# Kernel optimization log

Hardware: AMD Instinct MI355X
Metric: run time of the kernel (lower is better)

The kernel has to match this reference:

```python
import jax, jax.numpy as jnp
import numpy as np

# ---- static geometry derived from truncation (matches torch __init__) ----
T = 127
N_LAT_NH = T + 1                                   # 128 NH latitudes
LONS = [20 + 4 * i for i in range(N_LAT_NH)]       # octahedral reduced grid
CUMS = np.concatenate([[0], np.cumsum(np.array(LONS + LONS[::-1]))]).astype(int)
HZW_NH = np.minimum(4 + np.arange(N_LAT_NH), T)    # cubic truncation: m_max = nlon//4 - 1, capped at T
N_LATS_PER_M = np.array([(HZW_NH >= m).sum() for m in range(T + 1)])
L_SYM_FULL = (T + 3) // 2                          # 65 rows before dropping row 0
L_ANT = (T + 2) // 2                               # 64
N_VARS = 128
BATCH, ENS = 4, 1


def _tri_masks():
    """Zero-padded triangular structure of the per-m Legendre matrices."""
    sym = np.zeros((T + 1, L_SYM_FULL, N_LAT_NH), np.float32)
    ant = np.zeros((T + 1, L_ANT, N_LAT_NH), np.float32)
    for m in range(T + 1):
        n_lats = int(N_LATS_PER_M[m])
        ms = (T - m + 3) // 2
        off = L_SYM_FULL - ms
        sym[m, off:, N_LAT_NH - n_lats:] = 1.0
        if (m + 1) % 2 == 1:
            sym[m, off, :] = 0.0
        ma = (T - m + 2) // 2
        off = L_ANT - ma
        ant[m, off:, N_LAT_NH - n_lats:] = 1.0
        if m % 2 == 1:
            ant[m, off, :] = 0.0
    return sym[:, 1:, :], ant   # module drops first symmetric row -> [128,64,128]


def setup_inputs() -> dict:
    key = jax.random.key(0)
    k1, k2, k3 = jax.random.split(key, 3)
    n_grid = int(CUMS[-1])
    x = jax.random.normal(k1, (BATCH, ENS, n_grid, N_VARS), jnp.float32)
    sm, am = _tri_masks()
    # random stand-ins for (gaussian-weight-fused) Legendre polynomials, with the exact
    # triangular zero structure the module builds from ecTrans assets
    symmetric = jax.random.normal(k2, sm.shape, jnp.float32) * jnp.asarray(sm)
    antisymmetric = jax.random.normal(k3, am.shape, jnp.float32) * jnp.asarray(am)
    return {"x": x, "symmetric": symmetric, "antisymmetric": antisymmetric}


def reference(x, symmetric, antisymmetric):
    """Octahedral SHT forward: ragged longitudinal rfft -> hemispheric fold -> per-m Legendre matmuls.

    Returns spectrum [b, e, l, m, vars, 2] (real/imag stacked on last axis).
    """
    n_lat = 2 * N_LAT_NH
    north, south = [], []
    # loop is over structurally distinct (ragged) latitude ring lengths; NH lat i and its
    # SH mirror (lat n_lat-1-i) share nlon/truncation, so batch them in one FFT call.
    for i in range(N_LAT_NH):
        j = n_lat - 1 - i
        nlon = LONS[i]
        xn = x[:, :, CUMS[i]:CUMS[i + 1], :]           # [b,e,nlon,v]
        xs = x[:, :, CUMS[j]:CUMS[j + 1], :]
        xp = jnp.stack([xn, xs], axis=2)               # [b,e,2,nlon,v]
        f = jnp.fft.rfft(xp, axis=3) / nlon            # torch norm='forward'
        m_hi = int(HZW_NH[i]) + 1                      # keep m <= highest zonal wavenumber
        f = f[:, :, :, :m_hi, :]
        f = jnp.pad(f, ((0, 0), (0, 0), (0, 0), (0, T + 1 - m_hi), (0, 0)))
        north.append(f[:, :, 0])
        south.append(f[:, :, 1])                       # index i <-> lat n_lat-1-i: already pole-mirrored
    north = jnp.stack(north, axis=2)                   # [b,e,n_lat_nh,m,v] complex64
    south = jnp.stack(south, axis=2)
    # hemispheric symmetry of Legendre polynomials
    sym = north + south
    anti = north - south
    # per-m truncated Legendre contractions over NH latitudes (n)
    out_s = jnp.einsum('mln,benmv->belmv', symmetric, sym)     # [b,e,64,m,v]
    out_a = jnp.einsum('mln,benmv->belmv', antisymmetric, anti)
    # interleave symmetric (l-m even) and antisymmetric (l-m odd) rows -> full l axis (128)
    spec = jnp.stack([out_s, out_a], axis=3)
    b, e, L, _, M, V = spec.shape
    spec = spec.reshape(b, e, 2 * L, M, V)             # [b,e,l,m,v] complex, lower triangle zeros
    return jnp.stack([spec.real, spec.imag], axis=-1)  # real view [b,e,l,m,v,2]
```

## Files before the change

kernel.cpp:

```cpp
#include <hip/hip_runtime.h>
#include <math.h>

#define NGRID 70144
#define NV 128
#define JT 16
#define VS 64

typedef float f32x4 __attribute__((ext_vector_type(4)));
typedef short short8 __attribute__((ext_vector_type(8)));

__device__ __forceinline__ float4 f4add(float4 a, float4 b){ return make_float4(a.x+b.x, a.y+b.y, a.z+b.z, a.w+b.w); }
__device__ __forceinline__ float4 f4sub(float4 a, float4 b){ return make_float4(a.x-b.x, a.y-b.y, a.z-b.z, a.w-b.w); }

__device__ __forceinline__ unsigned f2bf(float f){
  unsigned u = __float_as_uint(f);
  return (u + 0x7FFFu + ((u>>16)&1u)) >> 16;
}
__device__ __forceinline__ float bf2f(unsigned h){ return __uint_as_float(h<<16); }

__device__ __forceinline__ long twoff_of(int i){
  long off = 0;
  for(int k=0;k<i;k++){
    int mh = (5+k < 128) ? (5+k) : 128;
    off += (long)mh * (long)(11 + 2*k);
  }
  return off;
}

__global__ void fill_tw(float* __restrict__ tw){
  int ring = blockIdx.x, mc = blockIdx.y;
  int N = 20 + 4*ring, H = N/2;
  int mhi = (5+ring < 128) ? (5+ring) : 128;
  int m0 = mc*32;
  if(m0 >= mhi) return;
  int m1 = (m0+32 < mhi) ? (m0+32) : mhi;
  long base = twoff_of(ring);
  int tot = (m1-m0)*(H+1);
  float invN = 1.0f / (float)N;
  for(int idx = threadIdx.x; idx < tot; idx += blockDim.x){
    int m = m0 + idx/(H+1);
    int j = idx % (H+1);
    int p = (m*j) % N;
    float th = 6.2831853071795864f * (float)p * invN;
    float sn, cs;
    __sincosf(th, &sn, &cs);
    long o = (base + (long)(m)*(H+1) + j)*2;
    tw[o]   = cs * invN;
    tw[o+1] = -sn * invN;
  }
}

__global__ __launch_bounds__(256) void dft_fold(const float* __restrict__ x,
                                                const float* __restrict__ tw,
                                                unsigned short* __restrict__ Gh,
                                                unsigned short* __restrict__ Gl){
  int ring = 127 - blockIdx.x;
  int mt = blockIdx.y;
  int b  = blockIdx.z >> 1;
  int vh = blockIdx.z & 1;
  int N = 20 + 4*ring, H = N/2, JC = H+1;
  int mhi = (5+ring < 128) ? (5+ring) : 128;
  int mbase = mt*32;
  if(mbase >= mhi) return;

  __shared__ __align__(16) float cS[JT][VS], sS[JT][VS], cA[JT][VS], sA[JT][VS];
  __shared__ __align__(16) float twl[JT][32][2];

  int tid = threadIdx.x;
  int vl = tid & 63;
  int mg = tid >> 6;
  int v  = vh*64 + vl;

  long twbase = twoff_of(ring);
  long offN = (long)ring*(2*ring+18);
  long a = ring+1;
  long offS = (long)NGRID - a*(2*a+18);
  const float* xn = x + ((long)b*NGRID + offN)*NV + vh*64;
  const float* xs = x + ((long)b*NGRID + offS)*NV + vh*64;

  float aSR[8], aSI[8], aAR[8], aAI[8];
  #pragma unroll
  for(int k=0;k<8;k++){ aSR[k]=0.f; aSI[k]=0.f; aAR[k]=0.f; aAI[k]=0.f; }

  int sjj = tid >> 4;
  int sv4 = (tid & 15) << 2;
  int tmp2 = (tid & 15) << 1;

  for(int j0=0; j0<JC; j0+=JT){
    __syncthreads();
    {
      int j = j0 + sjj;
      float4 z = make_float4(0.f,0.f,0.f,0.f);
      float4 nj=z, sj=z, np=z, sp=z;
      if(j < JC){
        nj = *(const float4*)&xn[(long)j*NV + sv4];
        sj = *(const float4*)&xs[(long)j*NV + sv4];
        if(j > 0 && j < H){
          int jp = N - j;
          np = *(const float4*)&xn[(long)jp*NV + sv4];
          sp = *(const float4*)&xs[(long)jp*NV + sv4];
        }
      }
      float4 e  = f4add(nj, sj);
      float4 o  = f4sub(nj, sj);
      float4 ep = f4add(np, sp);
      float4 op = f4sub(np, sp);
      *(float4*)&cS[sjj][sv4] = f4add(e, ep);
      *(float4*)&sS[sjj][sv4] = f4sub(e, ep);
      *(float4*)&cA[sjj][sv4] = f4add(o, op);
      *(float4*)&sA[sjj][sv4] = f4sub(o, op);
    }
    {
      int jsrc = j0 + sjj; if(jsrc > H) jsrc = H;
      int m0s = mbase + tmp2;     if(m0s > mhi-1) m0s = mhi-1;
      int m1s = mbase + tmp2 + 1; if(m1s > mhi-1) m1s = mhi-1;
      float2 t0 = *(const float2*)&tw[(twbase + (long)m0s*JC + jsrc)*2];
      float2 t1 = *(const float2*)&tw[(twbase + (long)m1s*JC + jsrc)*2];
      *(float4*)&twl[sjj][tmp2][0] = make_float4(t0.x, t0.y, t1.x, t1.y);
    }
    __syncthreads();
    int jlim = JC - j0; if(jlim > JT) jlim = JT;
    for(int jj=0; jj<jlim; jj++){
      float c_s = cS[jj][vl], s_s = sS[jj][vl], c_a = cA[jj][vl], s_a = sA[jj][vl];
      const float* twrow = &twl[jj][mg*8][0];
      #pragma unroll
      for(int k2=0; k2<4; k2++){
        float4 t4 = *(const float4*)&twrow[k2*4];
        aSR[2*k2]   += c_s*t4.x;  aSI[2*k2]   += s_s*t4.y;
        aAR[2*k2]   += c_a*t4.x;  aAI[2*k2]   += s_a*t4.y;
        aSR[2*k2+1] += c_s*t4.z;  aSI[2*k2+1] += s_s*t4.w;
        aAR[2*k2+1] += c_a*t4.z;  aAI[2*k2+1] += s_a*t4.w;
      }
    }
  }
  long gb = (long)ring*1024 + (long)b*256 + (long)v*2;
  #pragma unroll
  for(int k=0;k<8;k++){
    int m = mbase + mg*8 + k;
    if(m < mhi){
      long o = (long)m*131072 + gb;
      unsigned h0 = f2bf(aSR[k]), h1 = f2bf(aSI[k]);
      unsigned l0 = f2bf(aSR[k] - bf2f(h0)), l1 = f2bf(aSI[k] - bf2f(h1));
      *(unsigned*)&Gh[o] = h0 | (h1<<16);
      *(unsigned*)&Gl[o] = l0 | (l1<<16);
      unsigned a0 = f2bf(aAR[k]), a1 = f2bf(aAI[k]);
      unsigned b0 = f2bf(aAR[k] - bf2f(a0)), b1 = f2bf(aAI[k] - bf2f(a1));
      *(unsigned*)&Gh[o + 16777216L] = a0 | (a1<<16);
      *(unsigned*)&Gl[o + 16777216L] = b0 | (b1<<16);
    }
  }
}

__global__ void w_split(const float* __restrict__ Wsym, const float* __restrict__ Want,
                        unsigned short* __restrict__ Wh, unsigned short* __restrict__ Wl){
  long i = (long)blockIdx.x*256 + threadIdx.x;
  const float* W = (i < 1048576) ? Wsym : Want;
  float w = W[i & 1048575];
  unsigned h = f2bf(w);
  unsigned l = f2bf(w - bf2f(h));
  Wh[i] = (unsigned short)h;
  Wl[i] = (unsigned short)l;
}

__global__ __launch_bounds__(256) void legendre_mfma(const unsigned short* __restrict__ Wh,
                                                     const unsigned short* __restrict__ Wl,
                                                     const unsigned short* __restrict__ Gh,
                                                     const unsigned short* __restrict__ Gl,
                                                     float* __restrict__ out){
  int m = blockIdx.x, b = blockIdx.y, s = blockIdx.z;
  __shared__ __align__(16) unsigned short Bhs[8192];
  __shared__ __align__(16) unsigned short Bls[8192];
  int tid = threadIdx.x;
  int wave = tid >> 6, lane = tid & 63;
  int j = lane & 15, kb = lane >> 4;

  int kt0 = (m > 4) ? ((m-4) >> 5) : 0;

  const unsigned short* WA = Wh + (long)(s*128+m)*8192;
  const unsigned short* WB = Wl + (long)(s*128+m)*8192;
  long gBase = (long)(s*128+m)*131072 + (long)b*256 + tid;

  f32x4 acc[4][4];
  #pragma unroll
  for(int a=0;a<4;a++)
    #pragma unroll
    for(int q=0;q<4;q++) acc[a][q] = (f32x4){0.f,0.f,0.f,0.f};

  for(int kt=kt0; kt<4; ++kt){
    #pragma unroll
    for(int o=0;o<4;o++){
      long nb = gBase + (long)(kt*32 + o*8)*1024;
      unsigned p0=Gh[nb], p1=Gh[nb+1024], p2=Gh[nb+2048], p3=Gh[nb+3072],
               p4=Gh[nb+4096], p5=Gh[nb+5120], p6=Gh[nb+6144], p7=Gh[nb+7168];
      int4 pk = make_int4((int)(p0|(p1<<16)), (int)(p2|(p3<<16)),
                          (int)(p4|(p5<<16)), (int)(p6|(p7<<16)));
      *(int4*)&Bhs[tid*32 + ((o ^ (tid&3))<<3)] = pk;
      unsigned q0=Gl[nb], q1=Gl[nb+1024], q2=Gl[nb+2048], q3=Gl[nb+3072],
               q4=Gl[nb+4096], q5=Gl[nb+5120], q6=Gl[nb+6144], q7=Gl[nb+7168];
      int4 qk = make_int4((int)(q0|(q1<<16)), (int)(q2|(q3<<16)),
                          (int)(q4|(q5<<16)), (int)(q6|(q7<<16)));
      *(int4*)&Bls[tid*32 + ((o ^ (tid&3))<<3)] = qk;
    }
    __syncthreads();
    short8 ah[4], al[4];
    #pragma unroll
    for(int Mt=0;Mt<4;Mt++){
      const unsigned short* ap = WA + (Mt*16 + j)*128 + kt*32 + kb*8;
      ah[Mt] = *(const short8*)ap;
      al[Mt] = *(const short8*)(WB + (Mt*16 + j)*128 + kt*32 + kb*8);
    }
    #pragma unroll
    for(int nt=0;nt<4;nt++){
      int c = (wave*4+nt)*16 + j;
      short8 bh = *(short8*)&Bhs[c*32 + ((kb ^ (c&3))<<3)];
      short8 bl = *(short8*)&Bls[c*32 + ((kb ^ (c&3))<<3)];
      #pragma unroll
      for(int Mt=0;Mt<4;Mt++){
        acc[Mt][nt] = __builtin_amdgcn_mfma_f32_16x16x32_bf16(ah[Mt], bh, acc[Mt][nt], 0, 0, 0);
        acc[Mt][nt] = __builtin_amdgcn_mfma_f32_16x16x32_bf16(al[Mt], bh, acc[Mt][nt], 0, 0, 0);
        acc[Mt][nt] = __builtin_amdgcn_mfma_f32_16x16x32_bf16(ah[Mt], bl, acc[Mt][nt], 0, 0, 0);
      }
    }
    __syncthreads();
  }
  int r4 = (lane>>4)<<2;
  #pragma unroll
  for(int Mt=0;Mt<4;Mt++){
    #pragma unroll
    for(int nt=0;nt<4;nt++){
      int c = (wave*4+nt)*16 + j;
      #pragma unroll
      for(int reg=0;reg<4;reg++){
        int l = Mt*16 + r4 + reg;
        out[((long)(b*128 + 2*l + s)*128 + m)*256 + c] = acc[Mt][nt][reg];
      }
    }
  }
}

extern "C" void kernel_launch(void* const* d_in, const int* in_sizes, int n_in,
                              void* d_out, int out_size, void* d_ws, size_t ws_size,
                              hipStream_t stream) {
  const float* x    = (const float*)d_in[0];
  const float* Wsym = (const float*)d_in[1];
  const float* Want = (const float*)d_in[2];
  float* out = (float*)d_out;
  float* ws  = (float*)d_ws;

  long two = 0;
  for(int k=0;k<128;k++){ int mh = (5+k<128)?(5+k):128; two += (long)mh*(long)(11+2*k); }
  long GBASE = (two*2 + 255) & ~255L;

  float* tw = ws;
  unsigned short* Wh = (unsigned short*)ws;
  unsigned short* Wl = Wh + 2097152;
  unsigned short* Gh = (unsigned short*)(ws + GBASE);
  unsigned short* Gl = Gh + 33554432L;

  hipLaunchKernelGGL(fill_tw,       dim3(128,4),   dim3(256), 0, stream, tw);
  hipLaunchKernelGGL(dft_fold,      dim3(128,4,8), dim3(256), 0, stream, x, tw, Gh, Gl);
  hipLaunchKernelGGL(w_split,       dim3(8192),    dim3(256), 0, stream, Wsym, Want, Wh, Wl);
  hipLaunchKernelGGL(legendre_mfma, dim3(128,4,2), dim3(256), 0, stream, Wh, Wl, Gh, Gl, out);
}
```

Baseline: 417.1 us.

## Move ragged DFT onto bf16x3 MFMA and pack intermediate hi/lo spectra

Replaces the scalar FP32 DFT-fold kernel with an MFMA kernel. Twiddles are precomputed as padded bf16 hi/lo matrices, and the folded inputs are split into bf16 pairs and staged in swizzled LDS. The intermediate spectrum is stored as packed hi|lo 32-bit words in a new layout, so the Legendre kernel loads one word per element instead of two separate arrays. The aim is to move the DFT arithmetic from vector ALUs onto matrix cores and cut intermediate memory traffic, at the cost of more bf16 split arithmetic, padding waste on small rings and a larger twiddle table.

```diff
diff --git a/kernel.cpp b/kernel.cpp
--- a/kernel.cpp
+++ b/kernel.cpp
@@ -1,10 +1,8 @@
 #include <hip/hip_runtime.h>
-#include <math.h>
+#include <hip/hip_bf16.h>
 
 #define NGRID 70144
 #define NV 128
-#define JT 16
-#define VS 64
 
 typedef float f32x4 __attribute__((ext_vector_type(4)));
 typedef short short8 __attribute__((ext_vector_type(8)));
@@ -13,140 +11,178 @@
 __device__ __forceinline__ float4 f4sub(float4 a, float4 b){ return make_float4(a.x-b.x, a.y-b.y, a.z-b.z, a.w-b.w); }
 
 __device__ __forceinline__ unsigned f2bf(float f){
-  unsigned u = __float_as_uint(f);
-  return (u + 0x7FFFu + ((u>>16)&1u)) >> 16;
+  return (unsigned)__bfloat16_as_ushort(__float2bfloat16(f));
 }
 __device__ __forceinline__ float bf2f(unsigned h){ return __uint_as_float(h<<16); }
-
-__device__ __forceinline__ long twoff_of(int i){
+__device__ __forceinline__ unsigned packsplit(float f){
+  unsigned h = f2bf(f);
+  unsigned l = f2bf(f - bf2f(h));
+  return (h<<16) | l;
+}
+__device__ __forceinline__ int swzc(int c){ return (c ^ (c>>3)) & 7; }
+
+__device__ __forceinline__ void unpack_frag(int4 a, int4 b, short8 &bh, short8 &bl){
+  int h0 = (int)(((unsigned)a.x >> 16) | ((unsigned)a.y & 0xFFFF0000u));
+  int h1 = (int)(((unsigned)a.z >> 16) | ((unsigned)a.w & 0xFFFF0000u));
+  int h2 = (int)(((unsigned)b.x >> 16) | ((unsigned)b.y & 0xFFFF0000u));
+  int h3 = (int)(((unsigned)b.z >> 16) | ((unsigned)b.w & 0xFFFF0000u));
+  int l0 = (int)(((unsigned)a.x & 0xFFFFu) | ((unsigned)a.y << 16));
+  int l1 = (int)(((unsigned)a.z & 0xFFFFu) | ((unsigned)a.w << 16));
+  int l2 = (int)(((unsigned)b.x & 0xFFFFu) | ((unsigned)b.y << 16));
+  int l3 = (int)(((unsigned)b.z & 0xFFFFu) | ((unsigned)b.w << 16));
+  int4 H = make_int4(h0,h1,h2,h3), L = make_int4(l0,l1,l2,l3);
+  bh = *(short8*)&H; bl = *(short8*)&L;
+}
+
+__global__ void fill_tw(unsigned short* __restrict__ twA){
+  int ring = blockIdx.x, t = blockIdx.y;
+  int N = 20+4*ring, H = N/2, JC = H+1;
+  int mhi = (5+ring<128)?(5+ring):128;
+  int Mpad = ((mhi+15)>>4)<<4;
+  int Kpad = ((JC+31)>>5)<<5;
   long off = 0;
-  for(int k=0;k<i;k++){
-    int mh = (5+k < 128) ? (5+k) : 128;
-    off += (long)mh * (long)(11 + 2*k);
-  }
-  return off;
-}
-
-__global__ void fill_tw(float* __restrict__ tw){
-  int ring = blockIdx.x, mc = blockIdx.y;
-  int N = 20 + 4*ring, H = N/2;
-  int mhi = (5+ring < 128) ? (5+ring) : 128;
-  int m0 = mc*32;
-  if(m0 >= mhi) return;
-  int m1 = (m0+32 < mhi) ? (m0+32) : mhi;
-  long base = twoff_of(ring);
-  int tot = (m1-m0)*(H+1);
-  float invN = 1.0f / (float)N;
-  for(int idx = threadIdx.x; idx < tot; idx += blockDim.x){
-    int m = m0 + idx/(H+1);
-    int j = idx % (H+1);
-    int p = (m*j) % N;
-    float th = 6.2831853071795864f * (float)p * invN;
-    float sn, cs;
-    __sincosf(th, &sn, &cs);
-    long o = (base + (long)(m)*(H+1) + j)*2;
-    tw[o]   = cs * invN;
-    tw[o+1] = -sn * invN;
-  }
-}
-
-__global__ __launch_bounds__(256) void dft_fold(const float* __restrict__ x,
-                                                const float* __restrict__ tw,
-                                                unsigned short* __restrict__ Gh,
-                                                unsigned short* __restrict__ Gl){
-  int ring = 127 - blockIdx.x;
-  int mt = blockIdx.y;
-  int b  = blockIdx.z >> 1;
-  int vh = blockIdx.z & 1;
-  int N = 20 + 4*ring, H = N/2, JC = H+1;
-  int mhi = (5+ring < 128) ? (5+ring) : 128;
-  int mbase = mt*32;
-  if(mbase >= mhi) return;
-
-  __shared__ __align__(16) float cS[JT][VS], sS[JT][VS], cA[JT][VS], sA[JT][VS];
-  __shared__ __align__(16) float twl[JT][32][2];
+  for(int r=0;r<ring;r++){
+    int mh=(5+r<128)?(5+r):128, jc=11+2*r;
+    off += 4L*(((mh+15)>>4)<<4)*(((jc+31)>>5)<<5);
+  }
+  long MK = (long)Mpad*Kpad;
+  unsigned short* hiT = twA + off + (long)(t*2)*MK;
+  unsigned short* loT = hiT + MK;
+  float invN = 1.0f/(float)N;
+  for(long idx = threadIdx.x; idx < MK; idx += 256){
+    int m = (int)(idx / Kpad), j = (int)(idx % Kpad);
+    float val = 0.f;
+    if(m < mhi && j < JC){
+      int p = (m*j) % N;
+      float th = 6.2831853071795864f * (float)p * invN;
+      float sn, cs; __sincosf(th,&sn,&cs);
+      val = (t ? -sn : cs) * invN;
+    }
+    unsigned h = f2bf(val);
+    unsigned l = f2bf(val - bf2f(h));
+    hiT[idx] = (unsigned short)h;
+    loT[idx] = (unsigned short)l;
+  }
+}
+
+__global__ __launch_bounds__(256) void dft_mfma(const float* __restrict__ x,
+                                                const unsigned short* __restrict__ twA,
+                                                unsigned* __restrict__ Gp){
+  int bx = blockIdx.x;
+  int ring = 127 - (bx >> 1);
+  int type = bx & 1;
+  int b = blockIdx.y;
+  int N = 20+4*ring, H = N/2, JC = H+1;
+  int mhi = (5+ring<128)?(5+ring):128;
+  int Mt_n = (mhi+15)>>4;
+  int KT = (JC+31)>>5;
+  int Kpad = KT<<5;
+  int Mpad = Mt_n<<4;
+
+  long off = 0;
+  for(int r=0;r<ring;r++){
+    int mh=(5+r<128)?(5+r):128, jc=11+2*r;
+    off += 4L*(((mh+15)>>4)<<4)*(((jc+31)>>5)<<5);
+  }
+  long MK = (long)Mpad*Kpad;
+  const unsigned short* Ahi = twA + off + (long)(type*2)*MK;
+  const unsigned short* Alo = Ahi + MK;
+
+  const float* xn = x + ((long)b*NGRID + (long)ring*(2*ring+18))*NV;
+  long a1 = ring+1;
+  const float* xs = x + ((long)b*NGRID + (NGRID - a1*(2*a1+18)))*NV;
+
+  __shared__ __align__(16) unsigned Bp[8192];
 
   int tid = threadIdx.x;
-  int vl = tid & 63;
-  int mg = tid >> 6;
-  int v  = vh*64 + vl;
-
-  long twbase = twoff_of(ring);
-  long offN = (long)ring*(2*ring+18);
-  long a = ring+1;
-  long offS = (long)NGRID - a*(2*a+18);
-  const float* xn = x + ((long)b*NGRID + offN)*NV + vh*64;
-  const float* xs = x + ((long)b*NGRID + offS)*NV + vh*64;
-
-  float aSR[8], aSI[8], aAR[8], aAI[8];
-  #pragma unroll
-  for(int k=0;k<8;k++){ aSR[k]=0.f; aSI[k]=0.f; aAR[k]=0.f; aAI[k]=0.f; }
-
-  int sjj = tid >> 4;
-  int sv4 = (tid & 15) << 2;
-  int tmp2 = (tid & 15) << 1;
-
-  for(int j0=0; j0<JC; j0+=JT){
-    __syncthreads();
-    {
-      int j = j0 + sjj;
+  int jb = tid >> 5, vp = tid & 31;
+  int wave = tid >> 6, lane = tid & 63;
+  int jj = lane & 15, kb = lane >> 4;
+
+  f32x4 acc[8][4];
+  #pragma unroll
+  for(int Mt=0;Mt<8;Mt++)
+    #pragma unroll
+    for(int ct=0;ct<4;ct++) acc[Mt][ct] = (f32x4){0.f,0.f,0.f,0.f};
+
+  for(int kt=0; kt<KT; ++kt){
+    __syncthreads();
+    float4 fS[4], fA[4];
+    #pragma unroll
+    for(int dj=0;dj<4;dj++){
+      int j = kt*32 + jb*4 + dj;
       float4 z = make_float4(0.f,0.f,0.f,0.f);
       float4 nj=z, sj=z, np=z, sp=z;
       if(j < JC){
-        nj = *(const float4*)&xn[(long)j*NV + sv4];
-        sj = *(const float4*)&xs[(long)j*NV + sv4];
+        nj = *(const float4*)&xn[(long)j*NV + vp*4];
+        sj = *(const float4*)&xs[(long)j*NV + vp*4];
         if(j > 0 && j < H){
           int jp = N - j;
-          np = *(const float4*)&xn[(long)jp*NV + sv4];
-          sp = *(const float4*)&xs[(long)jp*NV + sv4];
+          np = *(const float4*)&xn[(long)jp*NV + vp*4];
+          sp = *(const float4*)&xs[(long)jp*NV + vp*4];
         }
       }
-      float4 e  = f4add(nj, sj);
-      float4 o  = f4sub(nj, sj);
-      float4 ep = f4add(np, sp);
-      float4 op = f4sub(np, sp);
-      *(float4*)&cS[sjj][sv4] = f4add(e, ep);
-      *(float4*)&sS[sjj][sv4] = f4sub(e, ep);
-      *(float4*)&cA[sjj][sv4] = f4add(o, op);
-      *(float4*)&sA[sjj][sv4] = f4sub(o, op);
-    }
-    {
-      int jsrc = j0 + sjj; if(jsrc > H) jsrc = H;
-      int m0s = mbase + tmp2;     if(m0s > mhi-1) m0s = mhi-1;
-      int m1s = mbase + tmp2 + 1; if(m1s > mhi-1) m1s = mhi-1;
-      float2 t0 = *(const float2*)&tw[(twbase + (long)m0s*JC + jsrc)*2];
-      float2 t1 = *(const float2*)&tw[(twbase + (long)m1s*JC + jsrc)*2];
-      *(float4*)&twl[sjj][tmp2][0] = make_float4(t0.x, t0.y, t1.x, t1.y);
-    }
-    __syncthreads();
-    int jlim = JC - j0; if(jlim > JT) jlim = JT;
-    for(int jj=0; jj<jlim; jj++){
-      float c_s = cS[jj][vl], s_s = sS[jj][vl], c_a = cA[jj][vl], s_a = sA[jj][vl];
-      const float* twrow = &twl[jj][mg*8][0];
+      float4 e  = f4add(nj, sj), o  = f4sub(nj, sj);
+      float4 ep = f4add(np, sp), op = f4sub(np, sp);
+      fS[dj] = type ? f4sub(e, ep) : f4add(e, ep);
+      fA[dj] = type ? f4sub(o, op) : f4add(o, op);
+    }
+    #pragma unroll
+    for(int dv=0;dv<4;dv++){
+      int c0 = (vp*4+dv)*2;
+      int4 wS = make_int4((int)packsplit(((const float*)&fS[0])[dv]),
+                          (int)packsplit(((const float*)&fS[1])[dv]),
+                          (int)packsplit(((const float*)&fS[2])[dv]),
+                          (int)packsplit(((const float*)&fS[3])[dv]));
+      *(int4*)&Bp[c0*32 + ((jb*4) ^ (swzc(c0)<<2))] = wS;
+      int c1 = c0 + 1;
+      int4 wA = make_int4((int)packsplit(((const float*)&fA[0])[dv]),
+                          (int)packsplit(((const float*)&fA[1])[dv]),
+                          (int)packsplit(((const float*)&fA[2])[dv]),
+                          (int)packsplit(((const float*)&fA[3])[dv]));
+      *(int4*)&Bp[c1*32 + ((jb*4) ^ (swzc(c1)<<2))] = wA;
+    }
+    __syncthreads();
+    short8 bh[4], bl[4];
+    #pragma unroll
+    for(int ct=0;ct<4;ct++){
+      int c = wave*64 + ct*16 + jj;
+      int sw = swzc(c)<<2;
+      int4 pa = *(const int4*)&Bp[c*32 + ((kb*8) ^ sw)];
+      int4 pb = *(const int4*)&Bp[c*32 + ((kb*8+4) ^ sw)];
+      unpack_frag(pa, pb, bh[ct], bl[ct]);
+    }
+    #pragma unroll
+    for(int Mt=0;Mt<8;Mt++){
+      if(Mt < Mt_n){
+        long ao = (long)(Mt*16 + jj)*Kpad + kt*32 + kb*8;
+        short8 ah = *(const short8*)&Ahi[ao];
+        short8 al = *(const short8*)&Alo[ao];
+        #pragma unroll
+        for(int ct=0;ct<4;ct++){
+          acc[Mt][ct] = __builtin_amdgcn_mfma_f32_16x16x32_bf16(ah, bh[ct], acc[Mt][ct], 0,0,0);
+          acc[Mt][ct] = __builtin_amdgcn_mfma_f32_16x16x32_bf16(al, bh[ct], acc[Mt][ct], 0,0,0);
+          acc[Mt][ct] = __builtin_amdgcn_mfma_f32_16x16x32_bf16(ah, bl[ct], acc[Mt][ct], 0,0,0);
+        }
+      }
+    }
+  }
+  #pragma unroll
+  for(int Mt=0;Mt<8;Mt++){
+    if(Mt < Mt_n){
       #pragma unroll
-      for(int k2=0; k2<4; k2++){
-        float4 t4 = *(const float4*)&twrow[k2*4];
-        aSR[2*k2]   += c_s*t4.x;  aSI[2*k2]   += s_s*t4.y;
-        aAR[2*k2]   += c_a*t4.x;  aAI[2*k2]   += s_a*t4.y;
-        aSR[2*k2+1] += c_s*t4.z;  aSI[2*k2+1] += s_s*t4.w;
-        aAR[2*k2+1] += c_a*t4.z;  aAI[2*k2+1] += s_a*t4.w;
-      }
-    }
-  }
-  long gb = (long)ring*1024 + (long)b*256 + (long)v*2;
-  #pragma unroll
-  for(int k=0;k<8;k++){
-    int m = mbase + mg*8 + k;
-    if(m < mhi){
-      long o = (long)m*131072 + gb;
-      unsigned h0 = f2bf(aSR[k]), h1 = f2bf(aSI[k]);
-      unsigned l0 = f2bf(aSR[k] - bf2f(h0)), l1 = f2bf(aSI[k] - bf2f(h1));
-      *(unsigned*)&Gh[o] = h0 | (h1<<16);
-      *(unsigned*)&Gl[o] = l0 | (l1<<16);
-      unsigned a0 = f2bf(aAR[k]), a1 = f2bf(aAI[k]);
-      unsigned b0 = f2bf(aAR[k] - bf2f(a0)), b1 = f2bf(aAI[k] - bf2f(a1));
-      *(unsigned*)&Gh[o + 16777216L] = a0 | (a1<<16);
-      *(unsigned*)&Gl[o + 16777216L] = b0 | (b1<<16);
+      for(int ct=0;ct<4;ct++){
+        int c = wave*64 + ct*16 + jj;
+        int s = c & 1, v = c >> 1;
+        #pragma unroll
+        for(int reg=0;reg<4;reg++){
+          int m = Mt*16 + (kb<<2) + reg;
+          if(m < mhi){
+            Gp[(long)((s*2+type)*128 + m)*65536 + (long)ring*512 + b*128 + v]
+              = packsplit(acc[Mt][ct][reg]);
+          }
+        }
+      }
     }
   }
 }
@@ -164,21 +200,20 @@
 
 __global__ __launch_bounds__(256) void legendre_mfma(const unsigned short* __restrict__ Wh,
                                                      const unsigned short* __restrict__ Wl,
-                                                     const unsigned short* __restrict__ Gh,
-                                                     const unsigned short* __restrict__ Gl,
+                                                     const unsigned* __restrict__ Gp,
                                                      float* __restrict__ out){
   int m = blockIdx.x, b = blockIdx.y, s = blockIdx.z;
-  __shared__ __align__(16) unsigned short Bhs[8192];
-  __shared__ __align__(16) unsigned short Bls[8192];
+  __shared__ __align__(16) unsigned Bp[8192];
   int tid = threadIdx.x;
   int wave = tid >> 6, lane = tid & 63;
-  int j = lane & 15, kb = lane >> 4;
+  int jj = lane & 15, kb = lane >> 4;
 
   int kt0 = (m > 4) ? ((m-4) >> 5) : 0;
 
   const unsigned short* WA = Wh + (long)(s*128+m)*8192;
   const unsigned short* WB = Wl + (long)(s*128+m)*8192;
-  long gBase = (long)(s*128+m)*131072 + (long)b*256 + tid;
+  int ri = tid & 1, v = tid >> 1;
+  long gC0 = (long)((s*2+ri)*128 + m)*65536 + (long)b*128 + v;
 
   f32x4 acc[4][4];
   #pragma unroll
@@ -186,49 +221,46 @@
     #pragma unroll
     for(int q=0;q<4;q++) acc[a][q] = (f32x4){0.f,0.f,0.f,0.f};
 
+  int swT = swzc(tid)<<2;
   for(int kt=kt0; kt<4; ++kt){
-    #pragma unroll
-    for(int o=0;o<4;o++){
-      long nb = gBase + (long)(kt*32 + o*8)*1024;
-      unsigned p0=Gh[nb], p1=Gh[nb+1024], p2=Gh[nb+2048], p3=Gh[nb+3072],
-               p4=Gh[nb+4096], p5=Gh[nb+5120], p6=Gh[nb+6144], p7=Gh[nb+7168];
-      int4 pk = make_int4((int)(p0|(p1<<16)), (int)(p2|(p3<<16)),
-                          (int)(p4|(p5<<16)), (int)(p6|(p7<<16)));
-      *(int4*)&Bhs[tid*32 + ((o ^ (tid&3))<<3)] = pk;
-      unsigned q0=Gl[nb], q1=Gl[nb+1024], q2=Gl[nb+2048], q3=Gl[nb+3072],
-               q4=Gl[nb+4096], q5=Gl[nb+5120], q6=Gl[nb+6144], q7=Gl[nb+7168];
-      int4 qk = make_int4((int)(q0|(q1<<16)), (int)(q2|(q3<<16)),
-                          (int)(q4|(q5<<16)), (int)(q6|(q7<<16)));
-      *(int4*)&Bls[tid*32 + ((o ^ (tid&3))<<3)] = qk;
-    }
-    __syncthreads();
-    short8 ah[4], al[4];
+    __syncthreads();
+    #pragma unroll
+    for(int k4=0;k4<32;k4+=4){
+      int4 w = make_int4((int)Gp[gC0 + (long)(kt*32+k4+0)*512],
+                         (int)Gp[gC0 + (long)(kt*32+k4+1)*512],
+                         (int)Gp[gC0 + (long)(kt*32+k4+2)*512],
+                         (int)Gp[gC0 + (long)(kt*32+k4+3)*512]);
+      *(int4*)&Bp[tid*32 + (k4 ^ swT)] = w;
+    }
+    __syncthreads();
+    short8 bh[4], bl[4];
+    #pragma unroll
+    for(int nt=0;nt<4;nt++){
+      int c = (wave*4+nt)*16 + jj;
+      int sw = swzc(c)<<2;
+      int4 pa = *(const int4*)&Bp[c*32 + ((kb*8) ^ sw)];
+      int4 pb = *(const int4*)&Bp[c*32 + ((kb*8+4) ^ sw)];
+      unpack_frag(pa, pb, bh[nt], bl[nt]);
+    }
     #pragma unroll
     for(int Mt=0;Mt<4;Mt++){
-      const unsigned short* ap = WA + (Mt*16 + j)*128 + kt*32 + kb*8;
-      ah[Mt] = *(const short8*)ap;
-      al[Mt] = *(const short8*)(WB + (Mt*16 + j)*128 + kt*32 + kb*8);
-    }
+      long ao = (long)(Mt*16 + jj)*128 + kt*32 + kb*8;
+      short8 ah = *(const short8*)&WA[ao];
+      short8 al = *(const short8*)&WB[ao];
+      #pragma unroll
+      for(int nt=0;nt<4;nt++){
+        acc[Mt][nt] = __builtin_amdgcn_mfma_f32_16x16x32_bf16(ah, bh[nt], acc[Mt][nt], 0,0,0);
+        acc[Mt][nt] = __builtin_amdgcn_mfma_f32_16x16x32_bf16(al, bh[nt], acc[Mt][nt], 0,0,0);
+        acc[Mt][nt] = __builtin_amdgcn_mfma_f32_16x16x32_bf16(ah, bl[nt], acc[Mt][nt], 0,0,0);
+      }
+    }
+  }
+  int r4 = (lane>>4)<<2;
+  #pragma unroll
+  for(int Mt=0;Mt<4;Mt++){
     #pragma unroll
     for(int nt=0;nt<4;nt++){
-      int c = (wave*4+nt)*16 + j;
-      short8 bh = *(short8*)&Bhs[c*32 + ((kb ^ (c&3))<<3)];
-      short8 bl = *(short8*)&Bls[c*32 + ((kb ^ (c&3))<<3)];
-      #pragma unroll
-      for(int Mt=0;Mt<4;Mt++){
-        acc[Mt][nt] = __builtin_amdgcn_mfma_f32_16x16x32_bf16(ah[Mt], bh, acc[Mt][nt], 0, 0, 0);
-        acc[Mt][nt] = __builtin_amdgcn_mfma_f32_16x16x32_bf16(al[Mt], bh, acc[Mt][nt], 0, 0, 0);
-        acc[Mt][nt] = __builtin_amdgcn_mfma_f32_16x16x32_bf16(ah[Mt], bl, acc[Mt][nt], 0, 0, 0);
-      }
-    }
-    __syncthreads();
-  }
-  int r4 = (lane>>4)<<2;
-  #pragma unroll
-  for(int Mt=0;Mt<4;Mt++){
-    #pragma unroll
-    for(int nt=0;nt<4;nt++){
-      int c = (wave*4+nt)*16 + j;
+      int c = (wave*4+nt)*16 + jj;
       #pragma unroll
       for(int reg=0;reg<4;reg++){
         int l = Mt*16 + r4 + reg;
@@ -245,20 +277,23 @@
   const float* Wsym = (const float*)d_in[1];
   const float* Want = (const float*)d_in[2];
   float* out = (float*)d_out;
-  float* ws  = (float*)d_ws;
-
-  long two = 0;
-  for(int k=0;k<128;k++){ int mh = (5+k<128)?(5+k):128; two += (long)mh*(long)(11+2*k); }
-  long GBASE = (two*2 + 255) & ~255L;
-
-  float* tw = ws;
-  unsigned short* Wh = (unsigned short*)ws;
+
+  long TWA = 0;
+  for(int r=0;r<128;r++){
+    int mh=(5+r<128)?(5+r):128, jc=11+2*r;
+    TWA += 4L*(((mh+15)/16)*16)*(((jc+31)/32)*32);
+  }
+  size_t gpOffB = (size_t)TWA*2;
+  if(gpOffB < 8388608) gpOffB = 8388608;
+  gpOffB = (gpOffB + 255) & ~(size_t)255;
+
+  unsigned short* twA = (unsigned short*)d_ws;
+  unsigned* Gp = (unsigned*)((char*)d_ws + gpOffB);
+  unsigned short* Wh = (unsigned short*)d_ws;
   unsigned short* Wl = Wh + 2097152;
-  unsigned short* Gh = (unsigned short*)(ws + GBASE);
-  unsigned short* Gl = Gh + 33554432L;
-
-  hipLaunchKernelGGL(fill_tw,       dim3(128,4),   dim3(256), 0, stream, tw);
-  hipLaunchKernelGGL(dft_fold,      dim3(128,4,8), dim3(256), 0, stream, x, tw, Gh, Gl);
+
+  hipLaunchKernelGGL(fill_tw,       dim3(128,2),   dim3(256), 0, stream, twA);
+  hipLaunchKernelGGL(dft_mfma,      dim3(256,4),   dim3(256), 0, stream, x, twA, Gp);
   hipLaunchKernelGGL(w_split,       dim3(8192),    dim3(256), 0, stream, Wsym, Want, Wh, Wl);
-  hipLaunchKernelGGL(legendre_mfma, dim3(128,4,2), dim3(256), 0, stream, Wh, Wl, Gh, Gl, out);
-}
+  hipLaunchKernelGGL(legendre_mfma, dim3(128,4,2), dim3(256), 0, stream, Wh, Wl, Gp, out);
+}
```

Result: no change. 415.3 us (-0.4%).
